# Kernel tuning notes

Measured on AMD Instinct MI355X. Metric: run time of the kernel, lower is better.

Reference implementation:

```python
import jax, jax.numpy as jnp
import numpy as np
from jax import lax

B = 1024          # batch
R = 100           # number of radical heads (TOP_RADICALS)


def _conv(x, w, b, padding):
    y = lax.conv_general_dilated(
        x, w, window_strides=(1, 1), padding=padding,
        dimension_numbers=('NCHW', 'OIHW', 'NCHW'))
    return y + b[None, :, None, None]


def _maxpool2(x):
    return lax.reduce_window(x, -jnp.inf, lax.max,
                             (1, 1, 2, 2), (1, 1, 2, 2), 'VALID')


def setup_inputs() -> dict:
    key = jax.random.key(0)
    ks = jax.random.split(key, 20)
    s = 0.05
    inp = {
        'x': jax.random.normal(ks[0], (B, 1, 98, 98), jnp.float32),
        'conv1_w': jax.random.normal(ks[1], (6, 1, 3, 3), jnp.float32) * s,
        'conv1_b': jnp.zeros((6,), jnp.float32),
        'conv2_w': jax.random.normal(ks[2], (4, 6, 6, 6), jnp.float32) * s,
        'conv2_b': jnp.zeros((4,), jnp.float32),
        'conv3_w': jax.random.normal(ks[3], (2, 4, 3, 3), jnp.float32) * s,
        'conv3_b': jnp.zeros((2,), jnp.float32),
        'fc1_w': jax.random.normal(ks[4], (200, 400), jnp.float32) * s,
        'fc1_b': jnp.zeros((400,), jnp.float32),
        'fc2_w': jax.random.normal(ks[5], (400, 200), jnp.float32) * s,
        'fc2_b': jnp.zeros((200,), jnp.float32),
        # all R per-radical heads stacked: Linear(200,140)->(140,84)->(84,42)->(42,4)
        'h1_w': jax.random.normal(ks[6], (R, 200, 140), jnp.float32) * s,
        'h1_b': jnp.zeros((R, 140), jnp.float32),
        'h2_w': jax.random.normal(ks[7], (R, 140, 84), jnp.float32) * s,
        'h2_b': jnp.zeros((R, 84), jnp.float32),
        'h3_w': jax.random.normal(ks[8], (R, 84, 42), jnp.float32) * s,
        'h3_b': jnp.zeros((R, 42), jnp.float32),
        'h4_w': jax.random.normal(ks[9], (R, 42, 4), jnp.float32) * s,
        'h4_b': jnp.zeros((R, 4), jnp.float32),
    }
    return inp


def reference(x, conv1_w, conv1_b, conv2_w, conv2_b, conv3_w, conv3_b,
              fc1_w, fc1_b, fc2_w, fc2_b,
              h1_w, h1_b, h2_w, h2_b, h3_w, h3_b, h4_w, h4_b):
    # conv trunk: conv -> relu -> maxpool, x3
    x = _maxpool2(jax.nn.relu(_conv(x, conv1_w, conv1_b, [(1, 1), (1, 1)])))  # [B,6,49,49]
    x = _maxpool2(jax.nn.relu(_conv(x, conv2_w, conv2_b, 'VALID')))           # [B,4,22,22]
    x = _maxpool2(jax.nn.relu(_conv(x, conv3_w, conv3_b, 'VALID')))           # [B,2,10,10]
    x = x.reshape(x.shape[0], -1)                                             # [B,200]
    # shared MLP trunk
    x = jax.nn.relu(x @ fc1_w + fc1_b)   # [B,400]
    x = jax.nn.relu(x @ fc2_w + fc2_b)   # [B,200]
    # R independent 4-layer heads, fused into batched einsums
    h = jax.nn.relu(jnp.einsum('bd,rdh->brh', x, h1_w) + h1_b)  # [B,R,140]
    h = jax.nn.relu(jnp.einsum('brd,rdh->brh', h, h2_w) + h2_b)  # [B,R,84]
    h = jax.nn.relu(jnp.einsum('brd,rdh->brh', h, h3_w) + h3_b)  # [B,R,42]
    h = jnp.einsum('brd,rdh->brh', h, h4_w) + h4_b               # [B,R,4]
    # torch.cat over heads along dim=1 == reshape [B, R*4]
    return h.reshape(h.shape[0], -1)
```

## Files before the change

kernel.cpp:

```cpp
#include <hip/hip_runtime.h>

#define NB 1024
#define NR 100

typedef _Float16 half_t;
typedef half_t f16x8 __attribute__((ext_vector_type(8)));
typedef float f32x4 __attribute__((ext_vector_type(4)));
typedef float f32x2 __attribute__((ext_vector_type(2)));

__device__ __forceinline__ int kmap2(int g, int j) {
    return g*4 + (j & 3) + ((j >> 2) << 4);
}

__device__ __forceinline__ f32x2 pkfma(f32x2 a, float s, f32x2 c) {
    return __builtin_elementwise_fma(a, (f32x2){s, s}, c);
}

#define GLDS(gsrc, ldst) \
    __builtin_amdgcn_global_load_lds( \
        (const __attribute__((address_space(1))) void*)(gsrc), \
        (__attribute__((address_space(3))) void*)(ldst), 16, 0, 0)

#define SWZ2(r, c) ((c) ^ ((((r) >> 1) & 3) << 3))

__global__ __launch_bounds__(256, 4) void conv12_k(const float* __restrict__ x,
        const float* __restrict__ wp1, const float* __restrict__ b1c,
        const float* __restrict__ wp2, const float* __restrict__ b2c,
        float* __restrict__ out) {
    __shared__ float img[56*57];
    __shared__ float c1o[6*27*32];
    const int blk = blockIdx.x;
    const int b  = blk >> 2;
    const int qy = (blk >> 1) & 1, qx = blk & 1;
    const int R0 = 44*qy - 1, C0 = 44*qx - 1;
    const int tid = threadIdx.x;
    const float* xb = x + (size_t)b * 9604;

    for (int i = tid; i < 56*56; i += 256) {
        const int rr = i / 56, cc = i - rr*56;
        const int gr = R0 + rr, gc = C0 + cc;
        float v = 0.f;
        if (gr >= 0 && gr < 98 && gc >= 0 && gc < 98) v = xb[gr*98 + gc];
        img[rr*57 + cc] = v;
    }
    __syncthreads();

    for (int pos = tid; pos < 729; pos += 256) {
        const int py = pos / 27, px = pos - py*27;
        float p[4][4];
        const float* base = img + (2*py)*57 + 2*px;
        #pragma unroll
        for (int u = 0; u < 4; ++u)
            #pragma unroll
            for (int v = 0; v < 4; ++v)
                p[u][v] = base[u*57 + v];
        f32x2 a2[3][4];
        #pragma unroll
        for (int g = 0; g < 3; ++g) {
            const f32x2 bv = *(const f32x2*)(b1c + g*2);
            a2[g][0] = a2[g][1] = a2[g][2] = a2[g][3] = bv;
        }
        #pragma unroll
        for (int ky = 0; ky < 3; ++ky)
            #pragma unroll
            for (int kx = 0; kx < 3; ++kx) {
                const int k = ky*3 + kx;
                const float q0 = p[ky  ][kx], q1 = p[ky  ][kx+1];
                const float q2 = p[ky+1][kx], q3 = p[ky+1][kx+1];
                #pragma unroll
                for (int g = 0; g < 3; ++g) {
                    const f32x2 wv = *(const f32x2*)(wp1 + (k*3+g)*2);
                    a2[g][0] = pkfma(wv, q0, a2[g][0]);
                    a2[g][1] = pkfma(wv, q1, a2[g][1]);
                    a2[g][2] = pkfma(wv, q2, a2[g][2]);
                    a2[g][3] = pkfma(wv, q3, a2[g][3]);
                }
            }
        #pragma unroll
        for (int g = 0; g < 3; ++g) {
            const float m0 = fmaxf(fmaxf(a2[g][0].x, a2[g][1].x),
                                   fmaxf(a2[g][2].x, a2[g][3].x));
            const float m1 = fmaxf(fmaxf(a2[g][0].y, a2[g][1].y),
                                   fmaxf(a2[g][2].y, a2[g][3].y));
            const int col = SWZ2(py, px);
            c1o[(g*2    )*864 + py*32 + col] = fmaxf(m0, 0.f);
            c1o[(g*2 + 1)*864 + py*32 + col] = fmaxf(m1, 0.f);
        }
    }
    __syncthreads();

    const int wv_ = tid >> 6;
    const int ocg = __builtin_amdgcn_readfirstlane(tid >> 7);
    const int unit = ((wv_ & 1) << 6) | (tid & 63);
    if (unit >= 121) return;
    const int py = unit / 11, px = unit - py*11;
    const int y0 = 2*py, x0 = 2*px;

    int aofs[7][4];
    #pragma unroll
    for (int u = 0; u < 7; ++u) {
        const int rr = y0 + u;
        #pragma unroll
        for (int vi = 0; vi < 3; ++vi)
            aofs[u][vi] = (rr*32 + SWZ2(rr, x0 + 2*vi)) * 4;
        aofs[u][3] = (rr*32 + SWZ2(rr, x0 + 6)) * 4;
    }

    const float* wg = wp2 + (size_t)ocg * 432;
    f32x2 acc2[2][2];
    {
        const f32x2 bv = *(const f32x2*)(b2c + ocg*2);
        acc2[0][0] = acc2[0][1] = acc2[1][0] = acc2[1][1] = bv;
    }

    #pragma unroll
    for (int ic = 0; ic < 6; ++ic) {
        const char* plane = (const char*)c1o + ic*3456;
        #pragma unroll
        for (int u = 0; u < 7; ++u) {
            float pr[7];
            *(f32x2*)&pr[0] = *(const f32x2*)(plane + aofs[u][0]);
            *(f32x2*)&pr[2] = *(const f32x2*)(plane + aofs[u][1]);
            *(f32x2*)&pr[4] = *(const f32x2*)(plane + aofs[u][2]);
            pr[6] = *(const float*)(plane + aofs[u][3]);
            #pragma unroll
            for (int dy = 0; dy < 2; ++dy) {
                const int ky = u - dy;
                if (ky < 0 || ky > 5) continue;
                #pragma unroll
                for (int kx = 0; kx < 6; ++kx) {
                    const f32x2 wv =
                        *(const f32x2*)(wg + (ic*36 + ky*6 + kx)*2);
                    acc2[dy][0] = pkfma(wv, pr[0+kx], acc2[dy][0]);
                    acc2[dy][1] = pkfma(wv, pr[1+kx], acc2[dy][1]);
                }
            }
        }
    }

    const int PY = qy*11 + py, PX = qx*11 + px;
    {
        const float m0 = fmaxf(fmaxf(acc2[0][0].x, acc2[0][1].x),
                               fmaxf(acc2[1][0].x, acc2[1][1].x));
        const float m1 = fmaxf(fmaxf(acc2[0][0].y, acc2[0][1].y),
                               fmaxf(acc2[1][0].y, acc2[1][1].y));
        out[(((size_t)b*4 + ocg*2    )*22 + PY)*22 + PX] = fmaxf(m0, 0.f);
        out[(((size_t)b*4 + ocg*2 + 1)*22 + PY)*22 + PX] = fmaxf(m1, 0.f);
    }
}

__global__ __launch_bounds__(256) void conv3_k(const float* __restrict__ in,
        const float* __restrict__ w, const float* __restrict__ bias,
        float* __restrict__ out) {
    __shared__ float sm[1936];
    const int b = blockIdx.x;
    const int tid = threadIdx.x;
    const float* src = in + (size_t)b * 1936;
    for (int i = tid; i < 484; i += 256)
        ((float4*)sm)[i] = ((const float4*)src)[i];
    __syncthreads();
    if (tid < 200) {
        const int c = tid / 100;
        const int rem = tid % 100;
        const int py = rem / 10, px = rem % 10;
        const int y0 = 2*py, x0 = 2*px;
        float a0, a1, a2, a3;
        a0 = a1 = a2 = a3 = bias[c];
        #pragma unroll
        for (int ic = 0; ic < 4; ++ic) {
            float p[4][4];
            const float* base = sm + ic*484 + y0*22 + x0;
            #pragma unroll
            for (int u = 0; u < 4; ++u)
                #pragma unroll
                for (int v = 0; v < 4; ++v)
                    p[u][v] = base[u*22 + v];
            #pragma unroll
            for (int ky = 0; ky < 3; ++ky) {
                #pragma unroll
                for (int kx = 0; kx < 3; ++kx) {
                    const float wv = w[(c*4 + ic)*9 + ky*3 + kx];
                    a0 = fmaf(wv, p[ky  ][kx  ], a0);
                    a1 = fmaf(wv, p[ky  ][kx+1], a1);
                    a2 = fmaf(wv, p[ky+1][kx  ], a2);
                    a3 = fmaf(wv, p[ky+1][kx+1], a3);
                }
            }
        }
        float m = fmaxf(fmaxf(a0, a1), fmaxf(a2, a3));
        out[(size_t)b*200 + tid] = fmaxf(m, 0.f);
    }
}

template<bool G0OUT>
__global__ __launch_bounds__(256, 4) void gemm_k(
        const float* __restrict__ A, int lda,
        const float* __restrict__ W, const float* __restrict__ bias,
        float* __restrict__ C, int ldc,
        int M, int N, int K,
        half_t* __restrict__ g0h, half_t* __restrict__ g0l) {
    __shared__ float As[32][132];
    __shared__ float Ws[32][64];
    const int m0 = blockIdx.y * 128;
    const int n0 = blockIdx.x * 64;
    const int tid = threadIdx.x;
    const int ti = tid >> 4, tj = tid & 15;
    float acc[8][4];
    #pragma unroll
    for (int i = 0; i < 8; ++i)
        #pragma unroll
        for (int j = 0; j < 4; ++j) acc[i][j] = 0.f;

    for (int k0 = 0; k0 < K; k0 += 32) {
        #pragma unroll
        for (int i = 0; i < 4; ++i) {
            const int f = tid + i*256;
            const int m = f >> 3, kg = f & 7;
            const int kk = kg*4;
            float4 v = make_float4(0.f, 0.f, 0.f, 0.f);
            if (k0 + kk < K)
                v = *(const float4*)(A + (long)(m0 + m)*lda + k0 + kk);
            As[kk+0][m] = v.x;
            As[kk+1][m] = v.y;
            As[kk+2][m] = v.z;
            As[kk+3][m] = v.w;
        }
        #pragma unroll
        for (int i = 0; i < 2; ++i) {
            const int f = tid + i*256;
            const int kk = f >> 4, cg = f & 15;
            const int n = n0 + cg*4;
            float4 v = make_float4(0.f, 0.f, 0.f, 0.f);
            if (k0 + kk < K) {
                const float* wp = W + (long)(k0 + kk)*N;
                if (n + 3 < N) v = *(const float4*)(wp + n);
                else {
                    if (n+0 < N) v.x = wp[n+0];
                    if (n+1 < N) v.y = wp[n+1];
                    if (n+2 < N) v.z = wp[n+2];
                }
            }
            *(float4*)&Ws[kk][cg*4] = v;
        }
        __syncthreads();
        #pragma unroll
        for (int kk = 0; kk < 32; ++kk) {
            float a[8], wv[4];
            *(float4*)&a[0] = *(const float4*)&As[kk][ti*8];
            *(float4*)&a[4] = *(const float4*)&As[kk][ti*8 + 4];
            *(float4*)&wv[0] = *(const float4*)&Ws[kk][tj*4];
            #pragma unroll
            for (int i = 0; i < 8; ++i)
                #pragma unroll
                for (int j = 0; j < 4; ++j)
                    acc[i][j] = fmaf(a[i], wv[j], acc[i][j]);
        }
        __syncthreads();
    }

    const int nb = n0 + tj*4;
    float bv[4] = {0.f, 0.f, 0.f, 0.f};
    #pragma unroll
    for (int e = 0; e < 4; ++e) if (nb + e < N) bv[e] = bias[nb + e];

    if (!G0OUT) {
        #pragma unroll
        for (int i = 0; i < 8; ++i) {
            const long m = m0 + ti*8 + i;
            if (nb + 3 < N) {
                float4 v;
                v.x = fmaxf(acc[i][0] + bv[0], 0.f);
                v.y = fmaxf(acc[i][1] + bv[1], 0.f);
                v.z = fmaxf(acc[i][2] + bv[2], 0.f);
                v.w = fmaxf(acc[i][3] + bv[3], 0.f);
                *(float4*)(C + m*(long)ldc + nb) = v;
            } else {
                #pragma unroll
                for (int j = 0; j < 4; ++j)
                    if (nb + j < N)
                        C[m*(long)ldc + nb + j] = fmaxf(acc[i][j] + bv[j], 0.f);
            }
        }
    } else {
        #pragma unroll
        for (int i = 0; i < 8; ++i) {
            const int m = m0 + ti*8 + i;
            #pragma unroll
            for (int j = 0; j < 4; ++j) {
                const int k = nb + j;
                if (k < N) {
                    const float v = fmaxf(acc[i][j] + bv[j], 0.f);
                    const half_t hi = (half_t)v;
                    const half_t lo = (half_t)(v - (float)hi);
                    const int kc = k >> 5, klo = k & 31;
                    const int h = klo >> 4, rm = klo & 15;
                    const int gg = rm >> 2, rr = rm & 3;
                    const size_t idx =
                        ((size_t)((m >> 4)*7 + kc)*64 + (gg << 4) + (m & 15))*8
                        + h*4 + rr;
                    g0h[idx] = hi;
                    g0l[idx] = lo;
                }
            }
        }
    }
}

__global__ __launch_bounds__(256) void wsplit_k(
        const float* __restrict__ w1, const float* __restrict__ w2,
        const float* __restrict__ w3, const float* __restrict__ w4,
        half_t* __restrict__ f1h, half_t* __restrict__ f1l,
        half_t* __restrict__ f2h, half_t* __restrict__ f2l,
        half_t* __restrict__ f3h, half_t* __restrict__ f3l,
        half_t* __restrict__ f4h, half_t* __restrict__ f4l,
        const float* __restrict__ c1w, const float* __restrict__ c2w,
        float* __restrict__ wp1, float* __restrict__ wp2) {
    __shared__ float lds[32*140];
    const int cx = blockIdx.x, r = blockIdx.y, tid = threadIdx.x;
    if (cx == 17) {
        if (r != 0) return;
        if (tid < 27) {
            const int k = tid / 3, g = tid - (tid/3)*3;
            wp1[tid*2+0] = c1w[(g*2+0)*9 + k];
            wp1[tid*2+1] = c1w[(g*2+1)*9 + k];
        }
        for (int i = tid; i < 432; i += 256) {
            const int ocg = i / 216, k = i - ocg*216;
            wp2[i*2+0] = c2w[(ocg*2+0)*216 + k];
            wp2[i*2+1] = c2w[(ocg*2+1)*216 + k];
        }
        return;
    }
    int K, N, KC, NF, kc;
    const float* src;
    half_t *dh, *dl;
    if (cx < 7)       { K=200; N=140; KC=7; NF=9; kc=cx;    src=w1; dh=f1h; dl=f1l; }
    else if (cx < 12) { K=140; N=84;  KC=5; NF=6; kc=cx-7;  src=w2; dh=f2h; dl=f2l; }
    else if (cx < 15) { K=84;  N=42;  KC=3; NF=3; kc=cx-12; src=w3; dh=f3h; dl=f3l; }
    else              { K=42;  N=4;   KC=2; NF=1; kc=cx-15; src=w4; dh=f4h; dl=f4l; }
    const float* sb = src + (size_t)r * K * N;
    for (int i = tid; i < 32*N; i += 256) {
        const int kk = i / N, n = i - kk*N;
        const int kg = kc*32 + kk;
        lds[kk*N + n] = (kg < K) ? sb[(size_t)kg*N + n] : 0.f;
    }
    __syncthreads();
    const size_t base = ((size_t)r*KC + kc)*NF*512;
    for (int e = tid; e < NF*512; e += 256) {
        const int nf = e >> 9, rem = e & 511;
        const int l = rem >> 3, j = rem & 7;
        const int g = l >> 4, c = l & 15;
        const int kl = kmap2(g, j);
        const int n = nf*16 + c;
        const float v = (n < N) ? lds[kl*N + n] : 0.f;
        const half_t hi = (half_t)v;
        const half_t lo = (half_t)(v - (float)hi);
        dh[base + (size_t)nf*512 + rem] = hi;
        dl[base + (size_t)nf*512 + rem] = lo;
    }
}

#define MFMA(a, b, c) __builtin_amdgcn_mfma_f32_16x16x32_f16(a, b, c, 0, 0, 0)

__global__ __launch_bounds__(256, 2) void head_k(
        const half_t* __restrict__ g0h, const half_t* __restrict__ g0l,
        const half_t* __restrict__ w1h, const half_t* __restrict__ w1l,
        const half_t* __restrict__ w2h, const half_t* __restrict__ w2l,
        const half_t* __restrict__ w3h, const half_t* __restrict__ w3l,
        const half_t* __restrict__ w4h, const half_t* __restrict__ w4l,
        const float* __restrict__ b1, const float* __restrict__ b2,
        const float* __restrict__ b3, const float* __restrict__ b4,
        float* __restrict__ out) {
    constexpr int CH = 18*512;
    __shared__ half_t wb[2*CH];
    __shared__ float bl[270];
    const int bid = blockIdx.x;
    const int cx  = bid & 7;
    const int kb  = bid >> 3;
    const int r   = ((kb >> 3) << 3) + cx;
    if (r >= NR) return;
    const int mt  = kb & 7;
    const int tid = threadIdx.x;
    if (tid < 140) bl[tid]       = b1[(size_t)r*140 + tid];
    if (tid < 84)  bl[140 + tid] = b2[(size_t)r*84  + tid];
    if (tid < 42)  bl[224 + tid] = b3[(size_t)r*42  + tid];
    if (tid < 4)   bl[266 + tid] = b4[(size_t)r*4   + tid];
    const int w = tid >> 6, l = tid & 63;
    const int g4 = ((l >> 4) & 3) * 4;
    const int mb0 = mt*8 + w*2;
    const size_t loff = (size_t)l * 8;

    auto stage1 = [&](int kc, half_t* buf) {
        const half_t* hs = w1h + ((size_t)r*7 + kc)*9*512;
        const half_t* ls = w1l + ((size_t)r*7 + kc)*9*512;
        #pragma unroll
        for (int p0 = 0; p0 < 3; ++p0) {
            const int p = w + p0*4;
            if (p < 9) {
                GLDS(hs + (size_t)p*512 + loff, buf + p*512);
                GLDS(ls + (size_t)p*512 + loff, buf + (9+p)*512);
            }
        }
    };
    auto stage2 = [&](int kc, half_t* buf) {
        const half_t* hs = w2h + ((size_t)r*5 + kc)*6*512;
        const half_t* ls = w2l + ((size_t)r*5 + kc)*6*512;
        #pragma unroll
        for (int p0 = 0; p0 < 2; ++p0) {
            const int p = w + p0*4;
            if (p < 6) {
                GLDS(hs + (size_t)p*512 + loff, buf + p*512);
                GLDS(ls + (size_t)p*512 + loff, buf + (6+p)*512);
            }
        }
    };
    auto stage3 = [&](int kc, half_t* buf) {
        const half_t* hs = w3h + ((size_t)r*3 + kc)*3*512;
        const half_t* ls = w3l + ((size_t)r*3 + kc)*3*512;
        if (w < 3) {
            GLDS(hs + (size_t)w*512 + loff, buf + w*512);
            GLDS(ls + (size_t)w*512 + loff, buf + (3+w)*512);
        }
    };

    f16x8 bhv[2][2], blv[2][2];
    stage1(0, wb);
    #pragma unroll
    for (int mb = 0; mb < 2; ++mb) {
        const size_t bo = ((size_t)(mb0 + mb)*7 + 0)*512 + loff;
        bhv[0][mb] = *(const f16x8*)(g0h + bo);
        blv[0][mb] = *(const f16x8*)(g0l + bo);
    }
    __syncthreads();
    f32x4 a1[2][9] = {};
    #pragma unroll
    for (int kc = 0; kc < 7; ++kc) {
        const half_t* cur = wb + (kc & 1)*CH;
        if (kc < 6) {
            stage1(kc+1, wb + ((kc+1) & 1)*CH);
            #pragma unroll
            for (int mb = 0; mb < 2; ++mb) {
                const size_t bo = ((size_t)(mb0 + mb)*7 + kc + 1)*512 + loff;
                bhv[(kc+1)&1][mb] = *(const f16x8*)(g0h + bo);
                blv[(kc+1)&1][mb] = *(const f16x8*)(g0l + bo);
            }
        } else {
            stage2(0, wb + CH);
        }
        #pragma unroll
        for (int nf = 0; nf < 9; ++nf) {
            const f16x8 wh = *(const f16x8*)(cur + nf*512 + loff);
            const f16x8 wl = *(const f16x8*)(cur + (9+nf)*512 + loff);
            #pragma unroll
            for (int mb = 0; mb < 2; ++mb) {
                a1[mb][nf] = MFMA(wh, bhv[kc&1][mb], a1[mb][nf]);
                a1[mb][nf] = MFMA(wh, blv[kc&1][mb], a1[mb][nf]);
                a1[mb][nf] = MFMA(wl, bhv[kc&1][mb], a1[mb][nf]);
            }
        }
        __syncthreads();
    }
    f16x8 b2h[2][5], b2l[2][5];
    #pragma unroll
    for (int kc = 0; kc < 5; ++kc)
        #pragma unroll
        for (int h = 0; h < 2; ++h) {
            const int nf = kc*2 + h;
            #pragma unroll
            for (int mb = 0; mb < 2; ++mb)
                #pragma unroll
                for (int rr = 0; rr < 4; ++rr) {
                    float v = 0.f;
                    if (nf < 9) {
                        const int n = nf*16 + g4 + rr;
                        v = (n < 140) ? fmaxf(a1[mb][nf][rr] + bl[n], 0.f) : 0.f;
                    }
                    const half_t hi = (half_t)v;
                    const half_t lo = (half_t)(v - (float)hi);
                    b2h[mb][kc][h*4+rr] = hi;
                    b2l[mb][kc][h*4+rr] = lo;
                }
        }
    f32x4 a2[2][6] = {};
    #pragma unroll
    for (int kc = 0; kc < 5; ++kc) {
        const half_t* cur = wb + (((kc+1) & 1))*CH;
        if (kc < 4) stage2(kc+1, wb + (kc & 1)*CH);
        else        stage3(0,    wb + (kc & 1)*CH);
        #pragma unroll
        for (int nf = 0; nf < 6; ++nf) {
            const f16x8 wh = *(const f16x8*)(cur + nf*512 + loff);
            const f16x8 wl = *(const f16x8*)(cur + (6+nf)*512 + loff);
            #pragma unroll
            for (int mb = 0; mb < 2; ++mb) {
                a2[mb][nf] = MFMA(wh, b2h[mb][kc], a2[mb][nf]);
                a2[mb][nf] = MFMA(wh, b2l[mb][kc], a2[mb][nf]);
                a2[mb][nf] = MFMA(wl, b2h[mb][kc], a2[mb][nf]);
            }
        }
        __syncthreads();
    }
    f16x8 b3h[2][3], b3l[2][3];
    #pragma unroll
    for (int kc = 0; kc < 3; ++kc)
        #pragma unroll
        for (int h = 0; h < 2; ++h) {
            const int nf = kc*2 + h;
            #pragma unroll
            for (int mb = 0; mb < 2; ++mb)
                #pragma unroll
                for (int rr = 0; rr < 4; ++rr) {
                    float v = 0.f;
                    if (nf < 6) {
                        const int n = nf*16 + g4 + rr;
                        v = (n < 84) ? fmaxf(a2[mb][nf][rr] + bl[140 + n], 0.f) : 0.f;
                    }
                    const half_t hi = (half_t)v;
                    const half_t lo = (half_t)(v - (float)hi);
                    b3h[mb][kc][h*4+rr] = hi;
                    b3l[mb][kc][h*4+rr] = lo;
                }
        }
    f32x4 a3[2][3] = {};
    #pragma unroll
    for (int kc = 0; kc < 3; ++kc) {
        const half_t* cur = wb + (kc & 1)*CH;
        if (kc < 2) stage3(kc+1, wb + ((kc+1) & 1)*CH);
        #pragma unroll
        for (int nf = 0; nf < 3; ++nf) {
            const f16x8 wh = *(const f16x8*)(cur + nf*512 + loff);
            const f16x8 wl = *(const f16x8*)(cur + (3+nf)*512 + loff);
            #pragma unroll
            for (int mb = 0; mb < 2; ++mb) {
                a3[mb][nf] = MFMA(wh, b3h[mb][kc], a3[mb][nf]);
                a3[mb][nf] = MFMA(wh, b3l[mb][kc], a3[mb][nf]);
                a3[mb][nf] = MFMA(wl, b3h[mb][kc], a3[mb][nf]);
            }
        }
        __syncthreads();
    }
    f16x8 b4h[2][2], b4l[2][2];
    #pragma unroll
    for (int kc = 0; kc < 2; ++kc)
        #pragma unroll
        for (int h = 0; h < 2; ++h) {
            const int nf = kc*2 + h;
            #pragma unroll
            for (int mb = 0; mb < 2; ++mb)
                #pragma unroll
                for (int rr = 0; rr < 4; ++rr) {
                    float v = 0.f;
                    if (nf < 3) {
                        const int n = nf*16 + g4 + rr;
                        v = (n < 42) ? fmaxf(a3[mb][nf][rr] + bl[224 + n], 0.f) : 0.f;
                    }
                    const half_t hi = (half_t)v;
                    const half_t lo = (half_t)(v - (float)hi);
                    b4h[mb][kc][h*4+rr] = hi;
                    b4l[mb][kc][h*4+rr] = lo;
                }
        }
    f32x4 a4[2] = {};
    #pragma unroll
    for (int kc = 0; kc < 2; ++kc) {
        const size_t wo = ((size_t)r*2 + kc)*512 + loff;
        const f16x8 wh = *(const f16x8*)(w4h + wo);
        const f16x8 wl = *(const f16x8*)(w4l + wo);
        #pragma unroll
        for (int mb = 0; mb < 2; ++mb) {
            a4[mb] = MFMA(wh, b4h[mb][kc], a4[mb]);
            a4[mb] = MFMA(wh, b4l[mb][kc], a4[mb]);
            a4[mb] = MFMA(wl, b4h[mb][kc], a4[mb]);
        }
    }
    if ((l >> 4) == 0) {
        #pragma unroll
        for (int mb = 0; mb < 2; ++mb) {
            const int b = (mb0 + mb)*16 + (l & 15);
            float4 o;
            o.x = a4[mb][0] + bl[266];
            o.y = a4[mb][1] + bl[267];
            o.z = a4[mb][2] + bl[268];
            o.w = a4[mb][3] + bl[269];
            *(float4*)(out + (size_t)b*400 + r*4) = o;
        }
    }
}

extern "C" void kernel_launch(void* const* d_in, const int* in_sizes, int n_in,
                              void* d_out, int out_size, void* d_ws, size_t ws_size,
                              hipStream_t stream) {
    const float* x    = (const float*)d_in[0];
    const float* c1w  = (const float*)d_in[1];
    const float* c1b  = (const float*)d_in[2];
    const float* c2w  = (const float*)d_in[3];
    const float* c2b  = (const float*)d_in[4];
    const float* c3w  = (const float*)d_in[5];
    const float* c3b  = (const float*)d_in[6];
    const float* fc1w = (const float*)d_in[7];
    const float* fc1b = (const float*)d_in[8];
    const float* fc2w = (const float*)d_in[9];
    const float* fc2b = (const float*)d_in[10];
    const float* h1w  = (const float*)d_in[11];
    const float* h1b  = (const float*)d_in[12];
    const float* h2w  = (const float*)d_in[13];
    const float* h2b  = (const float*)d_in[14];
    const float* h3w  = (const float*)d_in[15];
    const float* h3b  = (const float*)d_in[16];
    const float* h4w  = (const float*)d_in[17];
    const float* h4b  = (const float*)d_in[18];
    float* out = (float*)d_out;

    char* ws = (char*)d_ws;
    size_t o = 0;
    float* t2 = (float*)(ws + o); o += (size_t)NB*4*484*4;
    float* t3 = (float*)(ws + o); o += (size_t)NB*200*4;
    float* f1 = (float*)(ws + o); o += (size_t)NB*400*4;
    half_t* g0h = (half_t*)(ws + o); o += (size_t)64*7*512*2;
    half_t* g0l = (half_t*)(ws + o); o += (size_t)64*7*512*2;
    half_t* w1h = (half_t*)(ws + o); o += (size_t)NR*7*9*512*2;
    half_t* w1l = (half_t*)(ws + o); o += (size_t)NR*7*9*512*2;
    half_t* w2h = (half_t*)(ws + o); o += (size_t)NR*5*6*512*2;
    half_t* w2l = (half_t*)(ws + o); o += (size_t)NR*5*6*512*2;
    half_t* w3h = (half_t*)(ws + o); o += (size_t)NR*3*3*512*2;
    half_t* w3l = (half_t*)(ws + o); o += (size_t)NR*3*3*512*2;
    half_t* w4h = (half_t*)(ws + o); o += (size_t)NR*2*1*512*2;
    half_t* w4l = (half_t*)(ws + o); o += (size_t)NR*2*1*512*2;
    float* wp1 = (float*)(ws + o); o += 64*4;
    float* wp2 = (float*)(ws + o); o += 896*4;

    hipMemsetAsync(g0h, 0, (size_t)64*7*512*2*2, stream);

    wsplit_k<<<dim3(18, NR), 256, 0, stream>>>(h1w, h2w, h3w, h4w,
        w1h, w1l, w2h, w2l, w3h, w3l, w4h, w4l, c1w, c2w, wp1, wp2);

    conv12_k<<<NB*4, 256, 0, stream>>>(x, wp1, c1b, wp2, c2b, t2);
    conv3_k<<<NB, 256, 0, stream>>>(t2, c3w, c3b, t3);

    gemm_k<false><<<dim3(7, 8), 256, 0, stream>>>(
        t3, 200, fc1w, fc1b, f1, 400, NB, 400, 200, nullptr, nullptr);
    gemm_k<true><<<dim3(4, 8), 256, 0, stream>>>(
        f1, 400, fc2w, fc2b, nullptr, 0, NB, 200, 400, g0h, g0l);

    head_k<<<832, 256, 0, stream>>>(
        g0h, g0l, w1h, w1l, w2h, w2l, w3h, w3l, w4h, w4l,
        h1b, h2b, h3b, h4b, out);

    (void)in_sizes; (void)n_in; (void)out_size; (void)ws_size;
}
```

Before: 196.4 us.

## Store conv1 output in even/odd column-split LDS layout and raise occupancy

Replaces the swizzled 27x32-padded conv1 output buffer with a compact layout that splits columns by parity into separate even and odd planes of row stride 14 and 13. Conv2 then reads consecutive scalar words per row without swizzle address math and with fewer bank conflicts. The input image tile loses its padding column and is read with 2-wide vector loads. Together these shrink LDS use so launch bounds can target 5 blocks per CU instead of 4. The cost is more scalar LDS loads in conv2 and possible bank conflicts from the unpadded 56-stride image reads.

```diff
diff --git a/kernel.cpp b/kernel.cpp
--- a/kernel.cpp
+++ b/kernel.cpp
@@ -21,14 +21,13 @@
         (const __attribute__((address_space(1))) void*)(gsrc), \
         (__attribute__((address_space(3))) void*)(ldst), 16, 0, 0)
 
-#define SWZ2(r, c) ((c) ^ ((((r) >> 1) & 3) << 3))
-
-__global__ __launch_bounds__(256, 4) void conv12_k(const float* __restrict__ x,
+#define EOFF 2268
+__global__ __launch_bounds__(256, 5) void conv12_k(const float* __restrict__ x,
         const float* __restrict__ wp1, const float* __restrict__ b1c,
         const float* __restrict__ wp2, const float* __restrict__ b2c,
         float* __restrict__ out) {
-    __shared__ float img[56*57];
-    __shared__ float c1o[6*27*32];
+    __shared__ float img[56*56];
+    __shared__ float c1p[4374];
     const int blk = blockIdx.x;
     const int b  = blk >> 2;
     const int qy = (blk >> 1) & 1, qx = blk & 1;
@@ -41,19 +40,19 @@
         const int gr = R0 + rr, gc = C0 + cc;
         float v = 0.f;
         if (gr >= 0 && gr < 98 && gc >= 0 && gc < 98) v = xb[gr*98 + gc];
-        img[rr*57 + cc] = v;
+        img[i] = v;
     }
     __syncthreads();
 
     for (int pos = tid; pos < 729; pos += 256) {
         const int py = pos / 27, px = pos - py*27;
         float p[4][4];
-        const float* base = img + (2*py)*57 + 2*px;
-        #pragma unroll
-        for (int u = 0; u < 4; ++u)
-            #pragma unroll
-            for (int v = 0; v < 4; ++v)
-                p[u][v] = base[u*57 + v];
+        const float* base = img + (2*py)*56 + 2*px;
+        #pragma unroll
+        for (int u = 0; u < 4; ++u) {
+            *(f32x2*)&p[u][0] = *(const f32x2*)(base + u*56);
+            *(f32x2*)&p[u][2] = *(const f32x2*)(base + u*56 + 2);
+        }
         f32x2 a2[3][4];
         #pragma unroll
         for (int g = 0; g < 3; ++g) {
@@ -76,15 +75,19 @@
                     a2[g][3] = pkfma(wv, q3, a2[g][3]);
                 }
             }
+        const int par = px & 1, pi = px >> 1;
         #pragma unroll
         for (int g = 0; g < 3; ++g) {
             const float m0 = fmaxf(fmaxf(a2[g][0].x, a2[g][1].x),
                                    fmaxf(a2[g][2].x, a2[g][3].x));
             const float m1 = fmaxf(fmaxf(a2[g][0].y, a2[g][1].y),
                                    fmaxf(a2[g][2].y, a2[g][3].y));
-            const int col = SWZ2(py, px);
-            c1o[(g*2    )*864 + py*32 + col] = fmaxf(m0, 0.f);
-            c1o[(g*2 + 1)*864 + py*32 + col] = fmaxf(m1, 0.f);
+            const int e0 = par ? (EOFF + ((2*g    )*27 + py)*13 + pi)
+                               : (((2*g    )*27 + py)*14 + pi);
+            const int e1 = par ? (EOFF + ((2*g + 1)*27 + py)*13 + pi)
+                               : (((2*g + 1)*27 + py)*14 + pi);
+            c1p[e0] = fmaxf(m0, 0.f);
+            c1p[e1] = fmaxf(m1, 0.f);
         }
     }
     __syncthreads();
@@ -94,17 +97,7 @@
     const int unit = ((wv_ & 1) << 6) | (tid & 63);
     if (unit >= 121) return;
     const int py = unit / 11, px = unit - py*11;
-    const int y0 = 2*py, x0 = 2*px;
-
-    int aofs[7][4];
-    #pragma unroll
-    for (int u = 0; u < 7; ++u) {
-        const int rr = y0 + u;
-        #pragma unroll
-        for (int vi = 0; vi < 3; ++vi)
-            aofs[u][vi] = (rr*32 + SWZ2(rr, x0 + 2*vi)) * 4;
-        aofs[u][3] = (rr*32 + SWZ2(rr, x0 + 6)) * 4;
-    }
+    const int y0 = 2*py;
 
     const float* wg = wp2 + (size_t)ocg * 432;
     f32x2 acc2[2][2];
@@ -115,14 +108,15 @@
 
     #pragma unroll
     for (int ic = 0; ic < 6; ++ic) {
-        const char* plane = (const char*)c1o + ic*3456;
+        const float* pe0 = c1p + (ic*27 + y0)*14 + px;
+        const float* po0 = c1p + EOFF + (ic*27 + y0)*13 + px;
         #pragma unroll
         for (int u = 0; u < 7; ++u) {
+            const float* pe = pe0 + u*14;
+            const float* po = po0 + u*13;
             float pr[7];
-            *(f32x2*)&pr[0] = *(const f32x2*)(plane + aofs[u][0]);
-            *(f32x2*)&pr[2] = *(const f32x2*)(plane + aofs[u][1]);
-            *(f32x2*)&pr[4] = *(const f32x2*)(plane + aofs[u][2]);
-            pr[6] = *(const float*)(plane + aofs[u][3]);
+            pr[0] = pe[0]; pr[2] = pe[1]; pr[4] = pe[2]; pr[6] = pe[3];
+            pr[1] = po[0]; pr[3] = po[1]; pr[5] = po[2];
             #pragma unroll
             for (int dy = 0; dy < 2; ++dy) {
                 const int ky = u - dy;
```

Measured after the change: 195.1 us. No clear change (-0.7%).
